# Kernel tuning notes

Measured on AMD Instinct MI355X. Metric: run time of the kernel, lower is better.

The kernel has to match this reference:

```python
import jax, jax.numpy as jnp
import numpy as np

B, S, D, H, FF = 2, 2048, 768, 12, 3072
HD = D // H
NEG = -1e9


def _alibi_slopes(n_heads):
    start = 2.0 ** (-8.0 / n_heads)
    return np.array([start ** (i + 1) for i in range(n_heads)], dtype=np.float32)


def setup_inputs() -> dict:
    key = jax.random.key(0)
    ks = jax.random.split(key, 16)
    x = jax.random.normal(ks[0], (B, S, D), dtype=jnp.float32)
    # causal additive mask (seq, seq)
    mask = jnp.where(jnp.tril(jnp.ones((S, S), dtype=bool)), 0.0, NEG).astype(jnp.float32)
    # ALiBi bias (n_heads, seq, seq): slope * -(i - j) for j <= i
    slopes = jnp.asarray(_alibi_slopes(H))  # (H,)
    rel = jnp.arange(S)[None, :] - jnp.arange(S)[:, None]  # (S,S), j - i
    alibi_bias = (slopes[:, None, None] * rel[None, :, :]).astype(jnp.float32)
    sc = 0.02
    p = {
        'wq': jax.random.normal(ks[1], (D, D)) * sc, 'bq': jnp.zeros((D,)),
        'wk': jax.random.normal(ks[2], (D, D)) * sc, 'bk': jnp.zeros((D,)),
        'wv': jax.random.normal(ks[3], (D, D)) * sc, 'bv': jnp.zeros((D,)),
        'wo': jax.random.normal(ks[4], (D, D)) * sc, 'bo': jnp.zeros((D,)),
        'w1': jax.random.normal(ks[5], (FF, D)) * sc, 'b1': jnp.zeros((FF,)),
        'w2': jax.random.normal(ks[6], (D, FF)) * sc, 'b2': jnp.zeros((D,)),
        'g1': jnp.ones((D,)), 'be1': jnp.zeros((D,)),
        'g2': jnp.ones((D,)), 'be2': jnp.zeros((D,)),
    }
    return {'x': x, 'mask': mask, 'alibi_bias': alibi_bias, **p}


def _ln(x, g, b, eps=1e-5):
    mu = jnp.mean(x, axis=-1, keepdims=True)
    var = jnp.mean((x - mu) ** 2, axis=-1, keepdims=True)
    return (x - mu) * jax.lax.rsqrt(var + eps) * g + b


def reference(x, mask, alibi_bias, wq, bq, wk, bk, wv, bv, wo, bo,
              w1, b1, w2, b2, g1, be1, g2, be2):
    b, s, _ = x.shape
    def split_heads(t):
        return t.reshape(b, s, H, HD).transpose(0, 2, 1, 3)  # (B,H,S,HD)
    q = split_heads(x @ wq.T + bq)
    k = split_heads(x @ wk.T + bk)
    v = split_heads(x @ wv.T + bv)
    scores = jnp.einsum('bhqd,bhkd->bhqk', q, k) / jnp.sqrt(jnp.float32(HD))
    scores = scores + alibi_bias[None] + mask[None, None]
    attn = jax.nn.softmax(scores, axis=-1)
    out = jnp.einsum('bhqk,bhkd->bhqd', attn, v)
    out = out.transpose(0, 2, 1, 3).reshape(b, s, D)
    out = out @ wo.T + bo
    x = _ln(x + out, g1, be1)
    ff = jax.nn.relu(x @ w1.T + b1) @ w2.T + b2
    x = _ln(x + ff, g2, be2)
    return x
```

## Files before the change

kernel.cpp:

```cpp
#include <hip/hip_runtime.h>
#include <math.h>

#define BB   2
#define SS   2048
#define DD   768
#define HH   12
#define HDIM 64
#define FFD  3072

typedef __attribute__((ext_vector_type(8))) short bf16x8;
typedef __attribute__((ext_vector_type(4))) float f32x4;

__device__ __forceinline__ unsigned short f2bf(float f) {
  unsigned u = __float_as_uint(f);
  u += 0x7fffu + ((u >> 16) & 1u);
  return (unsigned short)(u >> 16);
}
__device__ __forceinline__ float bf2f(unsigned short s) {
  return __uint_as_float(((unsigned)s) << 16);
}

__device__ __forceinline__ void glb2lds16(const void* g, void* l) {
  __builtin_amdgcn_global_load_lds(
      (const __attribute__((address_space(1))) unsigned int*)g,
      (__attribute__((address_space(3))) unsigned int*)l, 16, 0, 0);
}

struct CastSegs {
  const float* src[7];
  unsigned short* dst[7];
  int cum[8];
};

__global__ __launch_bounds__(256) void cast_all_kernel(CastSegs segs, int total4) {
  int i = blockIdx.x * 256 + threadIdx.x;
  if (i >= total4) return;
  int s = 0;
  while (i >= segs.cum[s + 1]) ++s;
  int off = (i - segs.cum[s]) * 4;
  float4 f = *(const float4*)&segs.src[s][off];
  ushort4 o;
  o.x = f2bf(f.x); o.y = f2bf(f.y); o.z = f2bf(f.z); o.w = f2bf(f.w);
  *(ushort4*)&segs.dst[s][off] = o;
}

enum { EP_QKV3_BF16 = 0, EP_RELU_BF16 = 1, EP_F32_PART = 2, EP_BF16_PART = 3 };

template <int EPI, int SPLITK>
__global__ __launch_bounds__(256) void gemm_bt(
    const unsigned short* __restrict__ A, const unsigned short* __restrict__ W,
    const float* __restrict__ bias, const float* __restrict__ biasK,
    const float* __restrict__ biasV, void* __restrict__ C0,
    void* __restrict__ C1, void* __restrict__ C2,
    int M, int N, int K) {
  __shared__ unsigned short Alds[2][128 * 32];
  __shared__ unsigned short Blds[2][128 * 32];
  const int bm = blockIdx.y * 128, bn = blockIdx.x * 128;
  const int t = threadIdx.x;
  const int lane = t & 63;
  const int wid = t >> 6;
  const int wm = (wid >> 1) * 64, wn = (wid & 1) * 64;
  const int r16 = lane & 15, q4 = lane >> 4;
  const int klen = K / SPLITK;
  const int kbeg = (SPLITK > 1) ? blockIdx.z * klen : 0;
  const int kend = kbeg + klen;

  f32x4 acc[4][4] = {};

  auto stage = [&](int k0, int b) {
    #pragma unroll
    for (int l = 0; l < 2; ++l) {
      int c = t + l * 256;
      int row = c >> 2;
      int kq = (c & 3) ^ ((row >> 1) & 3);
      int base = ((t & 192) + l * 256) * 8;
      glb2lds16(&A[(size_t)(bm + row) * K + k0 + 8 * kq], &Alds[b][base]);
      glb2lds16(&W[(size_t)(bn + row) * K + k0 + 8 * kq], &Blds[b][base]);
    }
  };

  stage(kbeg, 0);
  int buf = 0;
  for (int k0 = kbeg; k0 < kend; k0 += 32) {
    __syncthreads();
    if (k0 + 32 < kend) stage(k0 + 32, buf ^ 1);
    bf16x8 af[4], bfv[4];
    #pragma unroll
    for (int i = 0; i < 4; ++i) {
      int row = wm + i * 16 + r16;
      af[i] = *(const bf16x8*)&Alds[buf][(row * 4 + (q4 ^ ((row >> 1) & 3))) * 8];
    }
    #pragma unroll
    for (int j = 0; j < 4; ++j) {
      int row = wn + j * 16 + r16;
      bfv[j] = *(const bf16x8*)&Blds[buf][(row * 4 + (q4 ^ ((row >> 1) & 3))) * 8];
    }
    #pragma unroll
    for (int i = 0; i < 4; ++i)
      #pragma unroll
      for (int j = 0; j < 4; ++j)
        acc[i][j] = __builtin_amdgcn_mfma_f32_16x16x32_bf16(af[i], bfv[j], acc[i][j], 0, 0, 0);
    buf ^= 1;
  }

  #pragma unroll
  for (int i = 0; i < 4; ++i) {
    #pragma unroll
    for (int j = 0; j < 4; ++j) {
      #pragma unroll
      for (int r = 0; r < 4; ++r) {
        int m = bm + wm + i * 16 + q4 * 4 + r;
        int n = bn + wn + j * 16 + r16;
        float val = acc[i][j][r];
        if (EPI == EP_QKV3_BF16) {
          int mat = (n >= 1536) ? 2 : (n >= 768 ? 1 : 0);
          int c = n - mat * 768;
          const float* bp = (mat == 0) ? bias : (mat == 1 ? biasK : biasV);
          val += bp[c];
          int b = m >> 11, s = m & 2047;
          int h = c >> 6, hd = c & 63;
          unsigned short* dst = (unsigned short*)(mat == 0 ? C0 : (mat == 1 ? C1 : C2));
          dst[(((size_t)b * HH + h) * SS + s) * HDIM + hd] = f2bf(val);
        } else if (EPI == EP_RELU_BF16) {
          val += bias[n];
          ((unsigned short*)C0)[(size_t)m * N + n] = f2bf(fmaxf(val, 0.f));
        } else if (EPI == EP_F32_PART) {
          ((float*)C0)[(size_t)blockIdx.z * M * N + (size_t)m * N + n] = val;
        } else {
          ((unsigned short*)C0)[(size_t)blockIdx.z * M * N + (size_t)m * N + n] = f2bf(val);
        }
      }
    }
  }
}

#define VSTR 72

__global__ __launch_bounds__(256) void attn5_kernel(
    const unsigned short* __restrict__ Q, const unsigned short* __restrict__ K,
    const unsigned short* __restrict__ V, unsigned short* __restrict__ Opart,
    float* __restrict__ Lpart) {
  __shared__ unsigned short Kl[2][64 * 64];
  __shared__ unsigned short Vt[2][64 * VSTR];
  __shared__ unsigned short Pl[4][16 * VSTR];

  const int qt = (SS / 64 - 1) - blockIdx.x;
  const int bh = blockIdx.y;
  const int z  = blockIdx.z;
  const int h = bh % HH;
  const int b = bh / HH;
  const int t = threadIdx.x;
  const int lane = t & 63, w = t >> 6;
  const int r16 = lane & 15, q4 = lane >> 4;
  const float k1 = 0.125f * 1.44269504f;
  const float slope2 = exp2f(-8.0f * (float)(h + 1) / 12.0f) * 1.44269504f;
  const int qg0 = qt * 64 + w * 16;

  const int nt = qt + 1;
  const int bsz = nt >> 2, rem = nt & 3;
  const int cnt = bsz + (z < rem ? 1 : 0);
  const int lo = z * bsz + (z < rem ? z : rem);
  const int hi = lo + cnt;

  bf16x8 qf[2];
  {
    const unsigned short* qbase = Q + ((size_t)bh * SS + qg0) * HDIM;
    #pragma unroll
    for (int ks = 0; ks < 2; ++ks)
      qf[ks] = *(const bf16x8*)(qbase + r16 * HDIM + ks * 32 + q4 * 8);
  }

  f32x4 O[4] = {};
  float rs[4] = {};

  const unsigned short* Kb = K + (size_t)bh * SS * HDIM;
  const unsigned short* Vb = V + (size_t)bh * SS * HDIM;
  const int kp = t & 31, dq = t >> 5;
  bf16x8 v0r, v1r;

  auto stageK = [&](int kt) {
    const unsigned short* kg = Kb + (size_t)kt * 64 * HDIM;
    #pragma unroll
    for (int l = 0; l < 2; ++l) {
      int c = t + l * 256;
      int key = c >> 3, kq = (c & 7) ^ (key & 7);
      glb2lds16(&kg[key * HDIM + 8 * kq], &Kl[kt & 1][((t & 192) + l * 256) * 8]);
    }
  };

  if (cnt > 0) {
    stageK(lo);
    const unsigned short* vg = Vb + (size_t)lo * 64 * HDIM;
    v0r = *(const bf16x8*)(vg + (2 * kp) * HDIM + dq * 8);
    v1r = *(const bf16x8*)(vg + (2 * kp + 1) * HDIM + dq * 8);
  }

  for (int kt = lo; kt < hi; ++kt) {
    unsigned short* Vtc = Vt[kt & 1];
    #pragma unroll
    for (int e = 0; e < 8; ++e) {
      unsigned u = ((unsigned)(unsigned short)v0r[e]) |
                   (((unsigned)(unsigned short)v1r[e]) << 16);
      *(unsigned*)&Vtc[(dq * 8 + e) * VSTR + 2 * kp] = u;
    }
    __syncthreads();
    if (kt + 1 < hi) {
      stageK(kt + 1);
      const unsigned short* vg = Vb + (size_t)(kt + 1) * 64 * HDIM;
      v0r = *(const bf16x8*)(vg + (2 * kp) * HDIM + dq * 8);
      v1r = *(const bf16x8*)(vg + (2 * kp + 1) * HDIM + dq * 8);
    }
    const unsigned short* Kt = Kl[kt & 1];

    f32x4 sc[4] = {};
    #pragma unroll
    for (int ks = 0; ks < 2; ++ks) {
      bf16x8 kf[4];
      #pragma unroll
      for (int jb = 0; jb < 4; ++jb) {
        int key = jb * 16 + r16;
        kf[jb] = *(const bf16x8*)&Kt[(key * 8 + ((ks * 4 + q4) ^ (key & 7))) * 8];
      }
      #pragma unroll
      for (int jb = 0; jb < 4; ++jb)
        sc[jb] = __builtin_amdgcn_mfma_f32_16x16x32_bf16(qf[ks], kf[jb], sc[jb], 0, 0, 0);
    }

    #pragma unroll
    for (int r = 0; r < 4; ++r) {
      int qrow = qg0 + q4 * 4 + r;
      int d0 = kt * 64 + r16 - qrow;
      #pragma unroll
      for (int jb = 0; jb < 4; ++jb) {
        int diff = d0 + jb * 16;
        float p = (diff <= 0) ? exp2f(sc[jb][r] * k1 + slope2 * (float)diff) : 0.f;
        rs[r] += p;
        Pl[w][(q4 * 4 + r) * VSTR + jb * 16 + r16] = f2bf(p);
      }
    }

    #pragma unroll
    for (int ks = 0; ks < 2; ++ks) {
      bf16x8 pf = *(const bf16x8*)&Pl[w][r16 * VSTR + ks * 32 + q4 * 8];
      bf16x8 vf[4];
      #pragma unroll
      for (int jb = 0; jb < 4; ++jb)
        vf[jb] = *(const bf16x8*)&Vtc[(jb * 16 + r16) * VSTR + ks * 32 + q4 * 8];
      #pragma unroll
      for (int jb = 0; jb < 4; ++jb)
        O[jb] = __builtin_amdgcn_mfma_f32_16x16x32_bf16(pf, vf[jb], O[jb], 0, 0, 0);
    }
  }

  #pragma unroll
  for (int r = 0; r < 4; ++r) {
    float lsum = rs[r];
    #pragma unroll
    for (int off = 1; off < 16; off <<= 1) lsum += __shfl_xor(lsum, off, 64);
    int qg = qg0 + q4 * 4 + r;
    if (r16 == 0)
      Lpart[((size_t)z * BB * HH + bh) * SS + qg] = lsum;
    unsigned short* ob = Opart + (size_t)z * BB * SS * DD +
                         ((size_t)b * SS + qg) * DD + h * HDIM;
    #pragma unroll
    for (int jb = 0; jb < 4; ++jb)
      ob[jb * 16 + r16] = f2bf(O[jb][r]);
  }
}

__global__ __launch_bounds__(256) void attn_combine_kernel(
    const unsigned short* __restrict__ Opart, const float* __restrict__ Lpart,
    unsigned short* __restrict__ at) {
  const size_t i = ((size_t)blockIdx.x * 256 + threadIdx.x) * 4;
  const int d = (int)(i % DD);
  const int sg = (int)(i / DD);
  const int b = sg >> 11, s = sg & 2047;
  const int h = d >> 6;
  const size_t zstr = (size_t)BB * SS * DD;
  float l = 0.f;
  #pragma unroll
  for (int zz = 0; zz < 4; ++zz)
    l += Lpart[((size_t)zz * BB * HH + b * HH + h) * SS + s];
  float inv = 1.f / l;
  float acc4[4] = {};
  #pragma unroll
  for (int zz = 0; zz < 4; ++zz) {
    ushort4 o4 = *(const ushort4*)&Opart[zz * zstr + i];
    acc4[0] += bf2f(o4.x); acc4[1] += bf2f(o4.y);
    acc4[2] += bf2f(o4.z); acc4[3] += bf2f(o4.w);
  }
  ushort4 r;
  r.x = f2bf(acc4[0] * inv); r.y = f2bf(acc4[1] * inv);
  r.z = f2bf(acc4[2] * inv); r.w = f2bf(acc4[3] * inv);
  *(ushort4*)&at[i] = r;
}

__device__ __forceinline__ void block_reduce2(float& s1, float& s2, int t) {
  __shared__ float red[8];
  #pragma unroll
  for (int off = 1; off < 64; off <<= 1) {
    s1 += __shfl_xor(s1, off, 64);
    s2 += __shfl_xor(s2, off, 64);
  }
  if ((t & 63) == 0) { red[(t >> 6) * 2] = s1; red[(t >> 6) * 2 + 1] = s2; }
  __syncthreads();
  s1 = red[0] + red[2] + red[4] + red[6];
  s2 = red[1] + red[3] + red[5] + red[7];
}

__global__ __launch_bounds__(256) void ln1_kernel(
    const float* __restrict__ x, const float* __restrict__ p,
    const float* __restrict__ bo, const float* __restrict__ g,
    const float* __restrict__ be, unsigned short* __restrict__ outb) {
  const int row = blockIdx.x, t = threadIdx.x;
  const size_t base = (size_t)row * DD;
  const size_t str = (size_t)BB * SS * DD;
  float v[3];
  float s1 = 0.f, s2 = 0.f;
  #pragma unroll
  for (int i = 0; i < 3; ++i) {
    int c = t + i * 256;
    v[i] = x[base + c] + p[base + c] + p[str + base + c] + bo[c];
    s1 += v[i]; s2 += v[i] * v[i];
  }
  block_reduce2(s1, s2, t);
  float mu = s1 * (1.0f / DD);
  float rstd = rsqrtf(s2 * (1.0f / DD) - mu * mu + 1e-5f);
  #pragma unroll
  for (int i = 0; i < 3; ++i) {
    int c = t + i * 256;
    outb[base + c] = f2bf((v[i] - mu) * rstd * g[c] + be[c]);
  }
}

__global__ __launch_bounds__(256) void ln2_kernel(
    const unsigned short* __restrict__ a, const unsigned short* __restrict__ f,
    const float* __restrict__ b2, const float* __restrict__ g,
    const float* __restrict__ be, float* __restrict__ out) {
  const int row = blockIdx.x, t = threadIdx.x;
  const size_t base = (size_t)row * DD;
  const size_t str = (size_t)BB * SS * DD;
  float v[3];
  float s1 = 0.f, s2 = 0.f;
  #pragma unroll
  for (int i = 0; i < 3; ++i) {
    int c = t + i * 256;
    size_t ix = base + c;
    v[i] = bf2f(a[ix]) + bf2f(f[ix]) + bf2f(f[str + ix]) +
           bf2f(f[2 * str + ix]) + bf2f(f[3 * str + ix]) + b2[c];
    s1 += v[i]; s2 += v[i] * v[i];
  }
  block_reduce2(s1, s2, t);
  float mu = s1 * (1.0f / DD);
  float rstd = rsqrtf(s2 * (1.0f / DD) - mu * mu + 1e-5f);
  #pragma unroll
  for (int i = 0; i < 3; ++i) {
    int c = t + i * 256;
    out[base + c] = (v[i] - mu) * rstd * g[c] + be[c];
  }
}

extern "C" void kernel_launch(void* const* d_in, const int* in_sizes, int n_in,
                              void* d_out, int out_size, void* d_ws, size_t ws_size,
                              hipStream_t stream) {
  const float* x   = (const float*)d_in[0];
  const float* wq  = (const float*)d_in[3];
  const float* bq  = (const float*)d_in[4];
  const float* wk  = (const float*)d_in[5];
  const float* bk  = (const float*)d_in[6];
  const float* wv  = (const float*)d_in[7];
  const float* bv  = (const float*)d_in[8];
  const float* wo  = (const float*)d_in[9];
  const float* bo  = (const float*)d_in[10];
  const float* w1  = (const float*)d_in[11];
  const float* b1  = (const float*)d_in[12];
  const float* w2  = (const float*)d_in[13];
  const float* b2  = (const float*)d_in[14];
  const float* g1  = (const float*)d_in[15];
  const float* be1 = (const float*)d_in[16];
  const float* g2  = (const float*)d_in[17];
  const float* be2 = (const float*)d_in[18];
  float* out = (float*)d_out;

  char* ws = (char*)d_ws;
  unsigned short* wqkvb = (unsigned short*)(ws + 0);
  unsigned short* wob   = (unsigned short*)(ws + 3538944);
  unsigned short* w1b   = (unsigned short*)(ws + 4718592);
  unsigned short* w2b   = (unsigned short*)(ws + 9437184);
  unsigned short* xb    = (unsigned short*)(ws + 14155776);
  unsigned short* qb    = (unsigned short*)(ws + 20456448);
  unsigned short* kb    = (unsigned short*)(ws + 26747904);
  unsigned short* vb    = (unsigned short*)(ws + 33039360);
  unsigned short* at    = (unsigned short*)(ws + 39330816);
  unsigned short* opart = (unsigned short*)(ws + 45622272);
  float*          lpart = (float*)(ws + 14155776);
  float*          pj    = (float*)(ws + 14155776);
  unsigned short* x1b   = (unsigned short*)(ws + 39330816);
  unsigned short* f1    = (unsigned short*)(ws + 45622272);
  unsigned short* f2b   = (unsigned short*)(ws + 14155776);

  const int M = BB * SS;
  dim3 blk(256);

  CastSegs cs;
  cs.src[0] = x;  cs.dst[0] = xb;
  cs.src[1] = wq; cs.dst[1] = wqkvb;
  cs.src[2] = wk; cs.dst[2] = wqkvb + DD * DD;
  cs.src[3] = wv; cs.dst[3] = wqkvb + 2 * DD * DD;
  cs.src[4] = wo; cs.dst[4] = wob;
  cs.src[5] = w1; cs.dst[5] = w1b;
  cs.src[6] = w2; cs.dst[6] = w2b;
  {
    int n[7] = {M * DD, DD * DD, DD * DD, DD * DD, DD * DD, FFD * DD, FFD * DD};
    int c = 0;
    for (int i = 0; i < 7; ++i) { cs.cum[i] = c; c += n[i] / 4; }
    cs.cum[7] = c;
    cast_all_kernel<<<dim3((c + 255) / 256), blk, 0, stream>>>(cs, c);
  }

  gemm_bt<EP_QKV3_BF16, 1><<<dim3(3 * DD / 128, M / 128, 1), blk, 0, stream>>>(
      xb, wqkvb, bq, bk, bv, qb, kb, vb, M, 3 * DD, DD);

  attn5_kernel<<<dim3(SS / 64, BB * HH, 4), blk, 0, stream>>>(qb, kb, vb, opart, lpart);
  attn_combine_kernel<<<dim3(M * DD / 1024), blk, 0, stream>>>(opart, lpart, at);

  gemm_bt<EP_F32_PART, 2><<<dim3(DD / 128, M / 128, 2), blk, 0, stream>>>(
      at, wob, nullptr, nullptr, nullptr, pj, nullptr, nullptr, M, DD, DD);

  ln1_kernel<<<dim3(M), blk, 0, stream>>>(x, pj, bo, g1, be1, x1b);

  gemm_bt<EP_RELU_BF16, 1><<<dim3(FFD / 128, M / 128, 1), blk, 0, stream>>>(
      x1b, w1b, b1, nullptr, nullptr, f1, nullptr, nullptr, M, FFD, DD);

  gemm_bt<EP_BF16_PART, 4><<<dim3(DD / 128, M / 128, 4), blk, 0, stream>>>(
      f1, w2b, nullptr, nullptr, nullptr, f2b, nullptr, nullptr, M, DD, FFD);

  ln2_kernel<<<dim3(M), blk, 0, stream>>>(x1b, f2b, b2, g2, be2, out);
}
```

Measured before the change: 492.2 us.

## Remap GEMM and attention block indices to keep shared data on one XCD

Replaces the 2D/3D grids of the GEMM and attention kernels with a 1D grid. Block IDs are decoded so that each of the 8 XCDs (round-robin dispatch on id&7) owns a contiguous set of column/split units or (batch-head, split) pairs. Blocks that reuse the same weight tiles or K/V data then share one XCD's L2 cache instead of being scattered across all of them. The cost is extra index arithmetic, and for some GEMM shapes padded blocks that return immediately, which can leave load imbalance across XCDs.

```diff
diff --git a/kernel.cpp b/kernel.cpp
--- a/kernel.cpp
+++ b/kernel.cpp
@@ -53,16 +53,27 @@
     const float* __restrict__ biasV, void* __restrict__ C0,
     void* __restrict__ C1, void* __restrict__ C2,
     int M, int N, int K) {
+  const int NX = N >> 7, NY = M >> 7, NU = NX * SPLITK;
+  const int id = blockIdx.x;
+  const int xcd = id & 7, slot = id >> 3;
+  const int u0 = (xcd * NU + 7) >> 3;
+  const int ucnt = (((xcd + 1) * NU + 7) >> 3) - u0;
+  const int iby = slot / ucnt;
+  if (iby >= NY) return;
+  const int unit = u0 + slot - iby * ucnt;
+  const int zz = unit / NX;
+  const int bxs = unit - zz * NX;
+  const int bm = iby * 128, bn = bxs * 128;
+
   __shared__ unsigned short Alds[2][128 * 32];
   __shared__ unsigned short Blds[2][128 * 32];
-  const int bm = blockIdx.y * 128, bn = blockIdx.x * 128;
   const int t = threadIdx.x;
   const int lane = t & 63;
   const int wid = t >> 6;
   const int wm = (wid >> 1) * 64, wn = (wid & 1) * 64;
   const int r16 = lane & 15, q4 = lane >> 4;
   const int klen = K / SPLITK;
-  const int kbeg = (SPLITK > 1) ? blockIdx.z * klen : 0;
+  const int kbeg = (SPLITK > 1) ? zz * klen : 0;
   const int kend = kbeg + klen;
 
   f32x4 acc[4][4] = {};
@@ -125,9 +136,9 @@
           val += bias[n];
           ((unsigned short*)C0)[(size_t)m * N + n] = f2bf(fmaxf(val, 0.f));
         } else if (EPI == EP_F32_PART) {
-          ((float*)C0)[(size_t)blockIdx.z * M * N + (size_t)m * N + n] = val;
+          ((float*)C0)[(size_t)zz * M * N + (size_t)m * N + n] = val;
         } else {
-          ((unsigned short*)C0)[(size_t)blockIdx.z * M * N + (size_t)m * N + n] = f2bf(val);
+          ((unsigned short*)C0)[(size_t)zz * M * N + (size_t)m * N + n] = f2bf(val);
         }
       }
     }
@@ -144,9 +155,14 @@
   __shared__ unsigned short Vt[2][64 * VSTR];
   __shared__ unsigned short Pl[4][16 * VSTR];
 
-  const int qt = (SS / 64 - 1) - blockIdx.x;
-  const int bh = blockIdx.y;
-  const int z  = blockIdx.z;
+  const int id = blockIdx.x;
+  const int xcd = id & 7, slot = id >> 3;
+  const int iu = slot % 12, qs = slot / 12;
+  const int unit = xcd * 12 + iu;
+  const int bh = unit >> 2;
+  const int z  = unit & 3;
+  const int qt = (SS / 64 - 1) - qs;
+
   const int h = bh % HH;
   const int b = bh / HH;
   const int t = threadIdx.x;
@@ -358,6 +374,15 @@
     int c = t + i * 256;
     out[base + c] = (v[i] - mu) * rstd * g[c] + be[c];
   }
+}
+
+static inline int grid1d_xcd(int NX, int NY, int SPLITK) {
+  int NU = NX * SPLITK, mx = 0;
+  for (int k = 0; k < 8; ++k) {
+    int c = ((((k + 1) * NU + 7) >> 3)) - (((k * NU + 7) >> 3));
+    if (c > mx) mx = c;
+  }
+  return 8 * mx * NY;
 }
 
 extern "C" void kernel_launch(void* const* d_in, const int* in_sizes, int n_in,
@@ -418,21 +443,21 @@
     cast_all_kernel<<<dim3((c + 255) / 256), blk, 0, stream>>>(cs, c);
   }
 
-  gemm_bt<EP_QKV3_BF16, 1><<<dim3(3 * DD / 128, M / 128, 1), blk, 0, stream>>>(
+  gemm_bt<EP_QKV3_BF16, 1><<<dim3(grid1d_xcd(18, 32, 1)), blk, 0, stream>>>(
       xb, wqkvb, bq, bk, bv, qb, kb, vb, M, 3 * DD, DD);
 
-  attn5_kernel<<<dim3(SS / 64, BB * HH, 4), blk, 0, stream>>>(qb, kb, vb, opart, lpart);
+  attn5_kernel<<<dim3(8 * 12 * 32), blk, 0, stream>>>(qb, kb, vb, opart, lpart);
   attn_combine_kernel<<<dim3(M * DD / 1024), blk, 0, stream>>>(opart, lpart, at);
 
-  gemm_bt<EP_F32_PART, 2><<<dim3(DD / 128, M / 128, 2), blk, 0, stream>>>(
+  gemm_bt<EP_F32_PART, 2><<<dim3(grid1d_xcd(6, 32, 2)), blk, 0, stream>>>(
       at, wob, nullptr, nullptr, nullptr, pj, nullptr, nullptr, M, DD, DD);
 
   ln1_kernel<<<dim3(M), blk, 0, stream>>>(x, pj, bo, g1, be1, x1b);
 
-  gemm_bt<EP_RELU_BF16, 1><<<dim3(FFD / 128, M / 128, 1), blk, 0, stream>>>(
+  gemm_bt<EP_RELU_BF16, 1><<<dim3(grid1d_xcd(24, 32, 1)), blk, 0, stream>>>(
       x1b, w1b, b1, nullptr, nullptr, f1, nullptr, nullptr, M, FFD, DD);
 
-  gemm_bt<EP_BF16_PART, 4><<<dim3(DD / 128, M / 128, 4), blk, 0, stream>>>(
+  gemm_bt<EP_BF16_PART, 4><<<dim3(grid1d_xcd(6, 32, 4)), blk, 0, stream>>>(
       f1, w2b, nullptr, nullptr, nullptr, f2b, nullptr, nullptr, M, DD, FFD);
 
   ln2_kernel<<<dim3(M), blk, 0, stream>>>(x1b, f2b, b2, g2, be2, out);
```

Result: faster. 461.5 us (-6.2%).
